# Performance work log

Measured on AMD Instinct MI355X. Metric: run time of the kernel, lower is better.

## Reference

```python
import jax, jax.numpy as jnp
import numpy as np
import math

# Dims chosen per input_specs
B, Q, S, T = 8, 64, 64, 64          # batch, queries, stat (segment) count, tokens per segment
H, DH = 8, 64                        # heads, head dim
NH = H * DH                          # num_hiddens = 512
STAT_K, TOKEN_K = 8, 16
NEG = -1e6


def setup_inputs() -> dict:
    key = jax.random.key(0)
    ks = jax.random.split(key, 11)
    f = lambda k, sh: jax.random.normal(k, sh, dtype=jnp.float32)
    w = lambda k: f(k, (NH, NH)) * 0.05  # Linear weights stored as [in, out]
    return {
        "queries": f(ks[0], (B, Q, NH)),
        "stat_keys": f(ks[1], (B, S, NH)),
        "token_keys": f(ks[2], (B * S, T, NH)),
        "values": f(ks[3], (B * S, T, NH)),
        "stat_valid_lens": jax.random.randint(ks[4], (B,), 1, S + 1, dtype=jnp.int32),
        "Wq_stat": w(ks[5]),
        "Wq_token": w(ks[6]),
        "Wk_stat": w(ks[7]),
        "Wk_token": w(ks[8]),
        "Wv": w(ks[9]),
        "Wo": w(ks[10]),
    }


def reference(queries, stat_keys, token_keys, values, stat_valid_lens,
              Wq_stat, Wq_token, Wk_stat, Wk_token, Wv, Wo):
    scale = 1.0 / math.sqrt(DH)

    def split_heads(x):  # [b, L, H*DH] -> [b, H, L, DH]
        b, L, _ = x.shape
        return x.reshape(b, L, H, DH).transpose(0, 2, 1, 3)

    q_stat = split_heads(queries @ Wq_stat)        # [B,H,Q,DH]
    q_tok = split_heads(queries @ Wq_token)        # [B,H,Q,DH]
    k_stat = split_heads(stat_keys @ Wk_stat)      # [B,H,S,DH]
    # token_keys/values come in as [B*S, T, size]; per-head layout [B,H,S,T,DH]
    k_tok = (token_keys @ Wk_token).reshape(B, S, T, H, DH).transpose(0, 3, 1, 2, 4)
    v = (values @ Wv).reshape(B, S, T, H, DH).transpose(0, 3, 1, 2, 4)

    # --- stat-level scores, valid-length mask, top-k sparsification, softmax ---
    stat_scores = jnp.einsum('bhqd,bhsd->bhqs', q_stat, k_stat) * scale  # [B,H,Q,S]
    valid = jnp.arange(S)[None, None, None, :] < stat_valid_lens[:, None, None, None]
    stat_scores = jnp.where(valid, stat_scores, NEG)
    k1 = min(S - 1, STAT_K)
    _, top_idx = jax.lax.top_k(stat_scores, k1)                           # [B,H,Q,k1]
    keep = jax.nn.one_hot(top_idx, S, dtype=stat_scores.dtype).sum(-2) > 0  # [B,H,Q,S]
    stat_w = jax.nn.softmax(jnp.where(keep, stat_scores, NEG), axis=-1)   # [B,H,Q,S]

    # --- token-level scores. NOTE: the original code computes torch.topk but then
    # overwrites with the LAST k2 positions (token_weights[:, :, -k2:] = ...), so the
    # token top-k result is dead code; we faithfully reproduce the last-k2 masking. ---
    tok_scores = jnp.einsum('bhqd,bhstd->bhsqt', q_tok, k_tok) * scale    # [B,H,S,Q,T]
    k2 = min(T - 1, TOKEN_K)
    last_mask = jnp.arange(T) >= (T - k2)
    tok_w = jax.nn.softmax(jnp.where(last_mask, tok_scores, NEG), axis=-1)
    tok_w = tok_w.transpose(0, 1, 3, 2, 4)                                # [B,H,Q,S,T]

    # --- combine hierarchy and attend over values ---
    comb = stat_w[..., None] * tok_w                                      # [B,H,Q,S,T]
    out = jnp.einsum('bhqst,bhstd->bhqd', comb, v)                        # [B,H,Q,DH]
    out = out.transpose(0, 2, 1, 3).reshape(B, Q, NH)
    return out @ Wo
```

## Files before the change

### kernel.cpp

```cpp
#include <hip/hip_runtime.h>
#include <hip/hip_bf16.h>

#define BB 8
#define QQ 64
#define SS 64
#define TT 64
#define HH 8
#define DH 64
#define NHID 512
#define STAT_K 8
#define TOKEN_K 16

typedef short bf16x8 __attribute__((ext_vector_type(8)));
typedef float f32x4 __attribute__((ext_vector_type(4)));

__device__ inline ushort f2bf_rne(float x) {
    union { float f; unsigned u; } v; v.f = x;
    unsigned r = v.u + 0x7fff + ((v.u >> 16) & 1);
    return (ushort)(r >> 16);
}
__device__ inline float bf2f(ushort h) {
    union { unsigned u; float f; } v; v.u = ((unsigned)h) << 16;
    return v.f;
}

__global__ __launch_bounds__(256) void conv_wT(
    const float* w0, const float* w1, const float* w2,
    const float* w3, const float* w4, const float* w5, ushort* dst)
{
    const float* srcs[6] = {w0, w1, w2, w3, w4, w5};
    const float* src = srcs[blockIdx.z];
    ushort* hi = dst + (size_t)blockIdx.z * 524288;
    ushort* lo = hi + 262144;
    __shared__ float t[32][33];
    const int c0 = blockIdx.x * 32, r0 = blockIdx.y * 32;
    const int tx = threadIdx.x & 31, ty = threadIdx.x >> 5;
    #pragma unroll
    for (int i = 0; i < 4; ++i)
        t[ty + 8 * i][tx] = src[(r0 + ty + 8 * i) * 512 + c0 + tx];
    __syncthreads();
    #pragma unroll
    for (int i = 0; i < 4; ++i) {
        float x = t[tx][ty + 8 * i];
        ushort h = f2bf_rne(x);
        int o = (c0 + ty + 8 * i) * 512 + r0 + tx;
        hi[o] = h;
        lo[o] = f2bf_rne(x - bf2f(h));
    }
}

__global__ void conv_split(const float* __restrict__ src,
                           ushort* __restrict__ hi, ushort* __restrict__ lo, int n)
{
    int i = blockIdx.x * blockDim.x + threadIdx.x;
    if (i < n) {
        float x = src[i];
        ushort h = f2bf_rne(x);
        hi[i] = h;
        lo[i] = f2bf_rne(x - bf2f(h));
    }
}

__global__ void conv_tok(const float* __restrict__ src, ushort* __restrict__ dst)
{
    int v = blockIdx.x * blockDim.x + threadIdx.x;
    int r = v >> 7, c = v & 127;
    int seg = r >> 4, tt = r & 15;
    const float4 x = *(const float4*)(src + (size_t)(seg * 64 + 48 + tt) * 512 + c * 4);
    ushort4 o;
    o.x = f2bf_rne(x.x); o.y = f2bf_rne(x.y);
    o.z = f2bf_rne(x.z); o.w = f2bf_rne(x.w);
    *(ushort4*)(dst + (size_t)v * 4) = o;
}

template <bool SPLIT, bool OUT_BF16>
__global__ __launch_bounds__(256) void gemm_mfma(
    const ushort* __restrict__ Ah, const ushort* __restrict__ Al,
    const ushort* __restrict__ Bh, const ushort* __restrict__ Bl,
    void* __restrict__ C, int M, int N, int K)
{
    __shared__ ushort As[SPLIT ? 2 : 1][64][40];
    __shared__ ushort Bs[SPLIT ? 2 : 1][64][40];
    const int tid = threadIdx.x;
    const int row0 = blockIdx.y * 64, col0 = blockIdx.x * 64;
    const int wave = tid >> 6, lane = tid & 63;
    const int wm = wave & 1, wn = wave >> 1;
    const int m16 = lane & 15, quad = lane >> 4;
    const int srow = tid >> 2, schunk = tid & 3;

    f32x4 acc[2][2];
    #pragma unroll
    for (int i = 0; i < 2; ++i)
        #pragma unroll
        for (int j = 0; j < 2; ++j)
            #pragma unroll
            for (int r = 0; r < 4; ++r) acc[i][j][r] = 0.f;

    for (int k0 = 0; k0 < K; k0 += 32) {
        const size_t aoff = (size_t)(row0 + srow) * K + k0 + schunk * 8;
        const size_t boff = (size_t)(col0 + srow) * K + k0 + schunk * 8;
        uint4 a_h = *(const uint4*)(Ah + aoff);
        uint4 b_h = *(const uint4*)(Bh + boff);
        *(uint4*)&As[0][srow][schunk * 8] = a_h;
        *(uint4*)&Bs[0][srow][schunk * 8] = b_h;
        if constexpr (SPLIT) {
            uint4 a_l = *(const uint4*)(Al + aoff);
            uint4 b_l = *(const uint4*)(Bl + boff);
            *(uint4*)&As[1][srow][schunk * 8] = a_l;
            *(uint4*)&Bs[1][srow][schunk * 8] = b_l;
        }
        __syncthreads();

        bf16x8 af[2], bf[2], afl[2], bfl[2];
        #pragma unroll
        for (int i = 0; i < 2; ++i) {
            af[i] = *(const bf16x8*)&As[0][wm * 32 + i * 16 + m16][quad * 8];
            bf[i] = *(const bf16x8*)&Bs[0][wn * 32 + i * 16 + m16][quad * 8];
            if constexpr (SPLIT) {
                afl[i] = *(const bf16x8*)&As[1][wm * 32 + i * 16 + m16][quad * 8];
                bfl[i] = *(const bf16x8*)&Bs[1][wn * 32 + i * 16 + m16][quad * 8];
            }
        }
        #pragma unroll
        for (int i = 0; i < 2; ++i)
            #pragma unroll
            for (int j = 0; j < 2; ++j) {
                acc[i][j] = __builtin_amdgcn_mfma_f32_16x16x32_bf16(af[i], bf[j], acc[i][j], 0, 0, 0);
                if constexpr (SPLIT) {
                    acc[i][j] = __builtin_amdgcn_mfma_f32_16x16x32_bf16(af[i], bfl[j], acc[i][j], 0, 0, 0);
                    acc[i][j] = __builtin_amdgcn_mfma_f32_16x16x32_bf16(afl[i], bf[j], acc[i][j], 0, 0, 0);
                }
            }
        __syncthreads();
    }

    #pragma unroll
    for (int i = 0; i < 2; ++i)
        #pragma unroll
        for (int j = 0; j < 2; ++j) {
            int r0 = row0 + wm * 32 + i * 16 + quad * 4;
            int c = col0 + wn * 32 + j * 16 + m16;
            #pragma unroll
            for (int reg = 0; reg < 4; ++reg) {
                float v = acc[i][j][reg];
                if constexpr (OUT_BF16)
                    ((ushort*)C)[(size_t)(r0 + reg) * N + c] = f2bf_rne(v);
                else
                    ((float*)C)[(size_t)(r0 + reg) * N + c] = v;
            }
        }
}

__global__ __launch_bounds__(64) void stat_topk(
    const float* __restrict__ q_stat, const float* __restrict__ k_stat,
    const int* __restrict__ valid_lens,
    int* __restrict__ sel_idx, float* __restrict__ sel_w)
{
    const int bid = blockIdx.x;
    const int b = bid >> 9;
    const int hq = bid & 511;
    const int h = hq >> 6;
    const int q = hq & 63;
    const int lane = threadIdx.x;

    __shared__ float sq[64];
    sq[lane] = q_stat[(b * QQ + q) * NHID + h * DH + lane];
    __syncthreads();

    const float4* kr = (const float4*)(k_stat + (b * SS + lane) * NHID + h * DH);
    const float4* sq4 = (const float4*)sq;
    float sc = 0.f;
    #pragma unroll
    for (int i = 0; i < 16; ++i) {
        float4 a = sq4[i], kk = kr[i];
        sc += a.x * kk.x + a.y * kk.y + a.z * kk.z + a.w * kk.w;
    }
    sc *= 0.125f;
    if (lane >= valid_lens[b]) sc = -1e6f;

    float my = sc;
    float mv[STAT_K];
    int   mi[STAT_K];
    #pragma unroll
    for (int j = 0; j < STAT_K; ++j) {
        float v = my;
        int idx = lane;
        #pragma unroll
        for (int off = 32; off > 0; off >>= 1) {
            float ov = __shfl_down(v, off);
            int   oi = __shfl_down(idx, off);
            if (ov > v || (ov == v && oi < idx)) { v = ov; idx = oi; }
        }
        v = __shfl(v, 0);
        idx = __shfl(idx, 0);
        mv[j] = v; mi[j] = idx;
        if (lane == idx) my = -3e38f;
    }
    float m0 = mv[0];
    float den = 0.f;
    float w[STAT_K];
    #pragma unroll
    for (int j = 0; j < STAT_K; ++j) { w[j] = __expf(mv[j] - m0); den += w[j]; }
    float inv = 1.f / den;
    if (lane < STAT_K) {
        sel_idx[bid * STAT_K + lane] = mi[lane];
        sel_w[bid * STAT_K + lane]   = w[lane] * inv;
    }
}

__global__ __launch_bounds__(64) void token_attend2(
    const float* __restrict__ q_tok, const ushort* __restrict__ k_tok,
    const ushort* __restrict__ v_proj, const int* __restrict__ sel_idx,
    const float* __restrict__ sel_w, float* __restrict__ ctx)
{
    const int bid = blockIdx.x;
    const int b = bid >> 9, h = (bid >> 6) & 7, q = bid & 63;
    const int lane = threadIdx.x;

    __shared__ float sq[64];
    __shared__ float ssc[16];
    __shared__ int   ssel[STAT_K];
    __shared__ float ssw[STAT_K];

    sq[lane] = q_tok[(size_t)(b * QQ + q) * NHID + h * DH + lane];
    if (lane < STAT_K) {
        ssel[lane] = sel_idx[bid * STAT_K + lane];
        ssw[lane]  = sel_w[bid * STAT_K + lane];
    }
    __syncthreads();

    const int t = lane >> 2, part = lane & 3;
    float acc = 0.f;

    for (int j = 0; j < STAT_K; ++j) {
        const int s = ssel[j];
        const float wseg = ssw[j];
        const size_t rowbase = (size_t)((b * SS + s) * TOKEN_K);

        const uint4* k4 = (const uint4*)(k_tok + (rowbase + t) * NHID + h * DH + part * 16);
        uint4 ka = k4[0], kb = k4[1];
        const float* qb = &sq[part * 16];
        float p = 0.f;
        p += qb[0]  * bf2f((ushort)(ka.x & 0xffff)) + qb[1]  * bf2f((ushort)(ka.x >> 16));
        p += qb[2]  * bf2f((ushort)(ka.y & 0xffff)) + qb[3]  * bf2f((ushort)(ka.y >> 16));
        p += qb[4]  * bf2f((ushort)(ka.z & 0xffff)) + qb[5]  * bf2f((ushort)(ka.z >> 16));
        p += qb[6]  * bf2f((ushort)(ka.w & 0xffff)) + qb[7]  * bf2f((ushort)(ka.w >> 16));
        p += qb[8]  * bf2f((ushort)(kb.x & 0xffff)) + qb[9]  * bf2f((ushort)(kb.x >> 16));
        p += qb[10] * bf2f((ushort)(kb.y & 0xffff)) + qb[11] * bf2f((ushort)(kb.y >> 16));
        p += qb[12] * bf2f((ushort)(kb.z & 0xffff)) + qb[13] * bf2f((ushort)(kb.z >> 16));
        p += qb[14] * bf2f((ushort)(kb.w & 0xffff)) + qb[15] * bf2f((ushort)(kb.w >> 16));
        p += __shfl_xor(p, 1);
        p += __shfl_xor(p, 2);
        if (part == 0) ssc[t] = p * 0.125f;
        __syncthreads();

        float m = ssc[0];
        #pragma unroll
        for (int tt = 1; tt < TOKEN_K; ++tt) m = fmaxf(m, ssc[tt]);
        float den = 0.f, wv[TOKEN_K];
        #pragma unroll
        for (int tt = 0; tt < TOKEN_K; ++tt) { wv[tt] = __expf(ssc[tt] - m); den += wv[tt]; }

        const ushort* vrow = v_proj + rowbase * NHID + h * DH + lane;
        float loc = 0.f;
        #pragma unroll
        for (int tt = 0; tt < TOKEN_K; ++tt) loc += wv[tt] * bf2f(vrow[tt * NHID]);
        acc += (wseg / den) * loc;
        __syncthreads();
    }

    ctx[(size_t)(b * QQ + q) * NHID + h * DH + lane] = acc;
}

extern "C" void kernel_launch(void* const* d_in, const int* in_sizes, int n_in,
                              void* d_out, int out_size, void* d_ws, size_t ws_size,
                              hipStream_t stream) {
    const float* queries    = (const float*)d_in[0];
    const float* stat_keys  = (const float*)d_in[1];
    const float* token_keys = (const float*)d_in[2];
    const float* values     = (const float*)d_in[3];
    const int*   valid_lens = (const int*)d_in[4];
    const float* Wq_stat    = (const float*)d_in[5];
    const float* Wq_token   = (const float*)d_in[6];
    const float* Wk_stat    = (const float*)d_in[7];
    const float* Wk_token   = (const float*)d_in[8];
    const float* Wv         = (const float*)d_in[9];
    const float* Wo         = (const float*)d_in[10];

    char* w = (char*)d_ws;
    ushort* wT      = (ushort*)(w + 0);
    ushort* q_hi    = (ushort*)(w + 6291456);
    ushort* q_lo    = q_hi + 262144;
    ushort* sk_hi   = (ushort*)(w + 7340032);
    ushort* sk_lo   = sk_hi + 262144;
    float*  q_stat  = (float*)(w + 8388608);
    float*  k_stat  = (float*)(w + 9437184);
    float*  q_tokf  = (float*)(w + 10485760);
    ushort* tok_hi  = (ushort*)(w + 11534336);
    ushort* k_tok   = (ushort*)(w + 19922944);
    ushort* v_projp = (ushort*)(w + 28311552);
    float*  ctx     = (float*)(w + 36700160);
    ushort* ctx_hi  = (ushort*)(w + 37748736);
    ushort* ctx_lo  = ctx_hi + 262144;
    float*  sel_w   = (float*)(w + 38797312);
    int*    sel_idx = (int*)(w + 38928384);

    ushort* wqs_h = wT + 0 * 524288, *wqs_l = wqs_h + 262144;
    ushort* wks_h = wT + 1 * 524288, *wks_l = wks_h + 262144;
    ushort* wqt_h = wT + 2 * 524288, *wqt_l = wqt_h + 262144;
    ushort* wkt_h = wT + 3 * 524288;
    ushort* wv_h  = wT + 4 * 524288;
    ushort* wo_h  = wT + 5 * 524288, *wo_l = wo_h + 262144;

    conv_wT<<<dim3(16, 16, 6), 256, 0, stream>>>(
        Wq_stat, Wk_stat, Wq_token, Wk_token, Wv, Wo, wT);
    conv_split<<<1024, 256, 0, stream>>>(queries, q_hi, q_lo, 262144);
    conv_split<<<1024, 256, 0, stream>>>(stat_keys, sk_hi, sk_lo, 262144);

    gemm_mfma<true, false><<<dim3(8, 8), 256, 0, stream>>>(
        q_hi, q_lo, wqs_h, wqs_l, q_stat, 512, 512, 512);
    gemm_mfma<true, false><<<dim3(8, 8), 256, 0, stream>>>(
        sk_hi, sk_lo, wks_h, wks_l, k_stat, 512, 512, 512);
    gemm_mfma<true, false><<<dim3(8, 8), 256, 0, stream>>>(
        q_hi, q_lo, wqt_h, wqt_l, q_tokf, 512, 512, 512);
    stat_topk<<<4096, 64, 0, stream>>>(q_stat, k_stat, valid_lens, sel_idx, sel_w);

    conv_tok<<<4096, 256, 0, stream>>>(token_keys, tok_hi);
    gemm_mfma<false, true><<<dim3(8, 128), 256, 0, stream>>>(
        tok_hi, nullptr, wkt_h, nullptr, k_tok, 8192, 512, 512);
    conv_tok<<<4096, 256, 0, stream>>>(values, tok_hi);
    gemm_mfma<false, true><<<dim3(8, 128), 256, 0, stream>>>(
        tok_hi, nullptr, wv_h, nullptr, v_projp, 8192, 512, 512);

    token_attend2<<<4096, 64, 0, stream>>>(q_tokf, k_tok, v_projp,
                                           sel_idx, sel_w, ctx);

    conv_split<<<1024, 256, 0, stream>>>(ctx, ctx_hi, ctx_lo, 262144);
    gemm_mfma<true, false><<<dim3(8, 8), 256, 0, stream>>>(
        ctx_hi, ctx_lo, wo_h, wo_l, (float*)d_out, 512, 512, 512);
}
```

Before: 270.0 us.

## Fuse conversion kernels into GEMMs and batch projection launches

Merges the weight transpose and the query/stat-key hi/lo splits into one launch, and batches the three split-precision projection GEMMs into a single grid using the z dimension. The token key/value conversion moves inside a combined GEMM that reads fp32 rows directly and converts them to bf16 while staging into shared memory. The ctx hi/lo split is folded into the attention epilogue. Together these cut the launch count from 14 to 6 and drop the intermediate bf16 token buffers and the fp32 ctx round trip. The cost is extra conversion work inside the GEMM inner loop and fp32 loads that read twice as many bytes.

```diff
diff --git a/kernel.cpp b/kernel.cpp
--- a/kernel.cpp
+++ b/kernel.cpp
@@ -24,63 +24,66 @@
     return v.f;
 }
 
-__global__ __launch_bounds__(256) void conv_wT(
+__global__ __launch_bounds__(256) void conv_all(
     const float* w0, const float* w1, const float* w2,
-    const float* w3, const float* w4, const float* w5, ushort* dst)
-{
-    const float* srcs[6] = {w0, w1, w2, w3, w4, w5};
-    const float* src = srcs[blockIdx.z];
-    ushort* hi = dst + (size_t)blockIdx.z * 524288;
-    ushort* lo = hi + 262144;
-    __shared__ float t[32][33];
-    const int c0 = blockIdx.x * 32, r0 = blockIdx.y * 32;
-    const int tx = threadIdx.x & 31, ty = threadIdx.x >> 5;
-    #pragma unroll
-    for (int i = 0; i < 4; ++i)
-        t[ty + 8 * i][tx] = src[(r0 + ty + 8 * i) * 512 + c0 + tx];
-    __syncthreads();
-    #pragma unroll
-    for (int i = 0; i < 4; ++i) {
-        float x = t[tx][ty + 8 * i];
-        ushort h = f2bf_rne(x);
-        int o = (c0 + ty + 8 * i) * 512 + r0 + tx;
-        hi[o] = h;
-        lo[o] = f2bf_rne(x - bf2f(h));
-    }
-}
-
-__global__ void conv_split(const float* __restrict__ src,
-                           ushort* __restrict__ hi, ushort* __restrict__ lo, int n)
-{
-    int i = blockIdx.x * blockDim.x + threadIdx.x;
-    if (i < n) {
-        float x = src[i];
-        ushort h = f2bf_rne(x);
-        hi[i] = h;
-        lo[i] = f2bf_rne(x - bf2f(h));
-    }
-}
-
-__global__ void conv_tok(const float* __restrict__ src, ushort* __restrict__ dst)
-{
-    int v = blockIdx.x * blockDim.x + threadIdx.x;
-    int r = v >> 7, c = v & 127;
-    int seg = r >> 4, tt = r & 15;
-    const float4 x = *(const float4*)(src + (size_t)(seg * 64 + 48 + tt) * 512 + c * 4);
-    ushort4 o;
-    o.x = f2bf_rne(x.x); o.y = f2bf_rne(x.y);
-    o.z = f2bf_rne(x.z); o.w = f2bf_rne(x.w);
-    *(ushort4*)(dst + (size_t)v * 4) = o;
-}
-
-template <bool SPLIT, bool OUT_BF16>
-__global__ __launch_bounds__(256) void gemm_mfma(
-    const ushort* __restrict__ Ah, const ushort* __restrict__ Al,
-    const ushort* __restrict__ Bh, const ushort* __restrict__ Bl,
-    void* __restrict__ C, int M, int N, int K)
-{
-    __shared__ ushort As[SPLIT ? 2 : 1][64][40];
-    __shared__ ushort Bs[SPLIT ? 2 : 1][64][40];
+    const float* w3, const float* w4, const float* w5,
+    const float* queries, const float* stat_keys,
+    ushort* wT, ushort* q_hi, ushort* q_lo, ushort* sk_hi, ushort* sk_lo)
+{
+    const int z = blockIdx.z;
+    if (z < 6) {
+        const float* srcs[6] = {w0, w1, w2, w3, w4, w5};
+        const float* src = srcs[z];
+        ushort* hi = wT + (size_t)z * 524288;
+        ushort* lo = hi + 262144;
+        __shared__ float t[32][33];
+        const int c0 = blockIdx.x * 32, r0 = blockIdx.y * 32;
+        const int tx = threadIdx.x & 31, ty = threadIdx.x >> 5;
+        #pragma unroll
+        for (int i = 0; i < 4; ++i)
+            t[ty + 8 * i][tx] = src[(r0 + ty + 8 * i) * 512 + c0 + tx];
+        __syncthreads();
+        #pragma unroll
+        for (int i = 0; i < 4; ++i) {
+            float x = t[tx][ty + 8 * i];
+            ushort h = f2bf_rne(x);
+            int o = (c0 + ty + 8 * i) * 512 + r0 + tx;
+            hi[o] = h;
+            lo[o] = f2bf_rne(x - bf2f(h));
+        }
+    } else {
+        const float* src = (z == 6) ? queries : stat_keys;
+        ushort* hi = (z == 6) ? q_hi : sk_hi;
+        ushort* lo = (z == 6) ? q_lo : sk_lo;
+        int base = (blockIdx.y * 16 + blockIdx.x) * 1024 + threadIdx.x * 4;
+        float4 x = *(const float4*)(src + base);
+        ushort4 h, l;
+        h.x = f2bf_rne(x.x); l.x = f2bf_rne(x.x - bf2f(h.x));
+        h.y = f2bf_rne(x.y); l.y = f2bf_rne(x.y - bf2f(h.y));
+        h.z = f2bf_rne(x.z); l.z = f2bf_rne(x.z - bf2f(h.z));
+        h.w = f2bf_rne(x.w); l.w = f2bf_rne(x.w - bf2f(h.w));
+        *(ushort4*)(hi + base) = h;
+        *(ushort4*)(lo + base) = l;
+    }
+}
+
+__global__ __launch_bounds__(256) void gemm_split3(
+    const ushort* __restrict__ q_hi, const ushort* __restrict__ q_lo,
+    const ushort* __restrict__ sk_hi, const ushort* __restrict__ sk_lo,
+    const ushort* __restrict__ wT,
+    float* __restrict__ q_stat, float* __restrict__ k_stat,
+    float* __restrict__ q_tokf)
+{
+    const int z = blockIdx.z;
+    const ushort* Ah = (z == 1) ? sk_hi : q_hi;
+    const ushort* Al = (z == 1) ? sk_lo : q_lo;
+    const ushort* Bh = wT + (size_t)z * 524288;
+    const ushort* Bl = Bh + 262144;
+    float* C = (z == 0) ? q_stat : (z == 1) ? k_stat : q_tokf;
+    const int K = 512, N = 512;
+
+    __shared__ ushort As[2][64][40];
+    __shared__ ushort Bs[2][64][40];
     const int tid = threadIdx.x;
     const int row0 = blockIdx.y * 64, col0 = blockIdx.x * 64;
     const int wave = tid >> 6, lane = tid & 63;
@@ -99,37 +102,27 @@
     for (int k0 = 0; k0 < K; k0 += 32) {
         const size_t aoff = (size_t)(row0 + srow) * K + k0 + schunk * 8;
         const size_t boff = (size_t)(col0 + srow) * K + k0 + schunk * 8;
-        uint4 a_h = *(const uint4*)(Ah + aoff);
-        uint4 b_h = *(const uint4*)(Bh + boff);
-        *(uint4*)&As[0][srow][schunk * 8] = a_h;
-        *(uint4*)&Bs[0][srow][schunk * 8] = b_h;
-        if constexpr (SPLIT) {
-            uint4 a_l = *(const uint4*)(Al + aoff);
-            uint4 b_l = *(const uint4*)(Bl + boff);
-            *(uint4*)&As[1][srow][schunk * 8] = a_l;
-            *(uint4*)&Bs[1][srow][schunk * 8] = b_l;
-        }
+        *(uint4*)&As[0][srow][schunk * 8] = *(const uint4*)(Ah + aoff);
+        *(uint4*)&Bs[0][srow][schunk * 8] = *(const uint4*)(Bh + boff);
+        *(uint4*)&As[1][srow][schunk * 8] = *(const uint4*)(Al + aoff);
+        *(uint4*)&Bs[1][srow][schunk * 8] = *(const uint4*)(Bl + boff);
         __syncthreads();
 
         bf16x8 af[2], bf[2], afl[2], bfl[2];
         #pragma unroll
         for (int i = 0; i < 2; ++i) {
-            af[i] = *(const bf16x8*)&As[0][wm * 32 + i * 16 + m16][quad * 8];
-            bf[i] = *(const bf16x8*)&Bs[0][wn * 32 + i * 16 + m16][quad * 8];
-            if constexpr (SPLIT) {
-                afl[i] = *(const bf16x8*)&As[1][wm * 32 + i * 16 + m16][quad * 8];
-                bfl[i] = *(const bf16x8*)&Bs[1][wn * 32 + i * 16 + m16][quad * 8];
-            }
+            af[i]  = *(const bf16x8*)&As[0][wm * 32 + i * 16 + m16][quad * 8];
+            bf[i]  = *(const bf16x8*)&Bs[0][wn * 32 + i * 16 + m16][quad * 8];
+            afl[i] = *(const bf16x8*)&As[1][wm * 32 + i * 16 + m16][quad * 8];
+            bfl[i] = *(const bf16x8*)&Bs[1][wn * 32 + i * 16 + m16][quad * 8];
         }
         #pragma unroll
         for (int i = 0; i < 2; ++i)
             #pragma unroll
             for (int j = 0; j < 2; ++j) {
                 acc[i][j] = __builtin_amdgcn_mfma_f32_16x16x32_bf16(af[i], bf[j], acc[i][j], 0, 0, 0);
-                if constexpr (SPLIT) {
-                    acc[i][j] = __builtin_amdgcn_mfma_f32_16x16x32_bf16(af[i], bfl[j], acc[i][j], 0, 0, 0);
-                    acc[i][j] = __builtin_amdgcn_mfma_f32_16x16x32_bf16(afl[i], bf[j], acc[i][j], 0, 0, 0);
-                }
+                acc[i][j] = __builtin_amdgcn_mfma_f32_16x16x32_bf16(af[i], bfl[j], acc[i][j], 0, 0, 0);
+                acc[i][j] = __builtin_amdgcn_mfma_f32_16x16x32_bf16(afl[i], bf[j], acc[i][j], 0, 0, 0);
             }
         __syncthreads();
     }
@@ -141,13 +134,143 @@
             int r0 = row0 + wm * 32 + i * 16 + quad * 4;
             int c = col0 + wn * 32 + j * 16 + m16;
             #pragma unroll
-            for (int reg = 0; reg < 4; ++reg) {
-                float v = acc[i][j][reg];
-                if constexpr (OUT_BF16)
-                    ((ushort*)C)[(size_t)(r0 + reg) * N + c] = f2bf_rne(v);
-                else
-                    ((float*)C)[(size_t)(r0 + reg) * N + c] = v;
+            for (int reg = 0; reg < 4; ++reg)
+                C[(size_t)(r0 + reg) * N + c] = acc[i][j][reg];
+        }
+}
+
+__global__ __launch_bounds__(256) void gemm_out(
+    const ushort* __restrict__ Ah, const ushort* __restrict__ Al,
+    const ushort* __restrict__ Bh, const ushort* __restrict__ Bl,
+    float* __restrict__ C)
+{
+    const int K = 512, N = 512;
+    __shared__ ushort As[2][64][40];
+    __shared__ ushort Bs[2][64][40];
+    const int tid = threadIdx.x;
+    const int row0 = blockIdx.y * 64, col0 = blockIdx.x * 64;
+    const int wave = tid >> 6, lane = tid & 63;
+    const int wm = wave & 1, wn = wave >> 1;
+    const int m16 = lane & 15, quad = lane >> 4;
+    const int srow = tid >> 2, schunk = tid & 3;
+
+    f32x4 acc[2][2];
+    #pragma unroll
+    for (int i = 0; i < 2; ++i)
+        #pragma unroll
+        for (int j = 0; j < 2; ++j)
+            #pragma unroll
+            for (int r = 0; r < 4; ++r) acc[i][j][r] = 0.f;
+
+    for (int k0 = 0; k0 < K; k0 += 32) {
+        const size_t aoff = (size_t)(row0 + srow) * K + k0 + schunk * 8;
+        const size_t boff = (size_t)(col0 + srow) * K + k0 + schunk * 8;
+        *(uint4*)&As[0][srow][schunk * 8] = *(const uint4*)(Ah + aoff);
+        *(uint4*)&Bs[0][srow][schunk * 8] = *(const uint4*)(Bh + boff);
+        *(uint4*)&As[1][srow][schunk * 8] = *(const uint4*)(Al + aoff);
+        *(uint4*)&Bs[1][srow][schunk * 8] = *(const uint4*)(Bl + boff);
+        __syncthreads();
+
+        bf16x8 af[2], bf[2], afl[2], bfl[2];
+        #pragma unroll
+        for (int i = 0; i < 2; ++i) {
+            af[i]  = *(const bf16x8*)&As[0][wm * 32 + i * 16 + m16][quad * 8];
+            bf[i]  = *(const bf16x8*)&Bs[0][wn * 32 + i * 16 + m16][quad * 8];
+            afl[i] = *(const bf16x8*)&As[1][wm * 32 + i * 16 + m16][quad * 8];
+            bfl[i] = *(const bf16x8*)&Bs[1][wn * 32 + i * 16 + m16][quad * 8];
+        }
+        #pragma unroll
+        for (int i = 0; i < 2; ++i)
+            #pragma unroll
+            for (int j = 0; j < 2; ++j) {
+                acc[i][j] = __builtin_amdgcn_mfma_f32_16x16x32_bf16(af[i], bf[j], acc[i][j], 0, 0, 0);
+                acc[i][j] = __builtin_amdgcn_mfma_f32_16x16x32_bf16(af[i], bfl[j], acc[i][j], 0, 0, 0);
+                acc[i][j] = __builtin_amdgcn_mfma_f32_16x16x32_bf16(afl[i], bf[j], acc[i][j], 0, 0, 0);
             }
+        __syncthreads();
+    }
+
+    #pragma unroll
+    for (int i = 0; i < 2; ++i)
+        #pragma unroll
+        for (int j = 0; j < 2; ++j) {
+            int r0 = row0 + wm * 32 + i * 16 + quad * 4;
+            int c = col0 + wn * 32 + j * 16 + m16;
+            #pragma unroll
+            for (int reg = 0; reg < 4; ++reg)
+                C[(size_t)(r0 + reg) * N + c] = acc[i][j][reg];
+        }
+}
+
+__global__ __launch_bounds__(256) void gemm_tok(
+    const float* __restrict__ token_keys, const float* __restrict__ values,
+    const ushort* __restrict__ wkt_h, const ushort* __restrict__ wv_h,
+    ushort* __restrict__ k_tok, ushort* __restrict__ v_proj)
+{
+    const int z = blockIdx.z;
+    const float* A = z ? values : token_keys;
+    const ushort* Bh = z ? wv_h : wkt_h;
+    ushort* C = z ? v_proj : k_tok;
+    const int K = 512, N = 512;
+
+    __shared__ ushort As[64][40];
+    __shared__ ushort Bs[64][40];
+    const int tid = threadIdx.x;
+    const int row0 = blockIdx.y * 64, col0 = blockIdx.x * 64;
+    const int wave = tid >> 6, lane = tid & 63;
+    const int wm = wave & 1, wn = wave >> 1;
+    const int m16 = lane & 15, quad = lane >> 4;
+    const int srow = tid >> 2, schunk = tid & 3;
+
+    const int r = row0 + srow;
+    const size_t arow = (size_t)((r >> 4) * 64 + 48 + (r & 15)) * K;
+
+    f32x4 acc[2][2];
+    #pragma unroll
+    for (int i = 0; i < 2; ++i)
+        #pragma unroll
+        for (int j = 0; j < 2; ++j)
+            #pragma unroll
+            for (int rr = 0; rr < 4; ++rr) acc[i][j][rr] = 0.f;
+
+    for (int k0 = 0; k0 < K; k0 += 32) {
+        const float* ap = A + arow + k0 + schunk * 8;
+        float4 x0 = ((const float4*)ap)[0];
+        float4 x1 = ((const float4*)ap)[1];
+        ushort4 h0, h1;
+        h0.x = f2bf_rne(x0.x); h0.y = f2bf_rne(x0.y);
+        h0.z = f2bf_rne(x0.z); h0.w = f2bf_rne(x0.w);
+        h1.x = f2bf_rne(x1.x); h1.y = f2bf_rne(x1.y);
+        h1.z = f2bf_rne(x1.z); h1.w = f2bf_rne(x1.w);
+        *(ushort4*)&As[srow][schunk * 8] = h0;
+        *(ushort4*)&As[srow][schunk * 8 + 4] = h1;
+        *(uint4*)&Bs[srow][schunk * 8] =
+            *(const uint4*)(Bh + (size_t)(col0 + srow) * K + k0 + schunk * 8);
+        __syncthreads();
+
+        bf16x8 af[2], bf[2];
+        #pragma unroll
+        for (int i = 0; i < 2; ++i) {
+            af[i] = *(const bf16x8*)&As[wm * 32 + i * 16 + m16][quad * 8];
+            bf[i] = *(const bf16x8*)&Bs[wn * 32 + i * 16 + m16][quad * 8];
+        }
+        #pragma unroll
+        for (int i = 0; i < 2; ++i)
+            #pragma unroll
+            for (int j = 0; j < 2; ++j)
+                acc[i][j] = __builtin_amdgcn_mfma_f32_16x16x32_bf16(af[i], bf[j], acc[i][j], 0, 0, 0);
+        __syncthreads();
+    }
+
+    #pragma unroll
+    for (int i = 0; i < 2; ++i)
+        #pragma unroll
+        for (int j = 0; j < 2; ++j) {
+            int r0 = row0 + wm * 32 + i * 16 + quad * 4;
+            int c = col0 + wn * 32 + j * 16 + m16;
+            #pragma unroll
+            for (int reg = 0; reg < 4; ++reg)
+                C[(size_t)(r0 + reg) * N + c] = f2bf_rne(acc[i][j][reg]);
         }
 }
 
@@ -211,7 +334,8 @@
 __global__ __launch_bounds__(64) void token_attend2(
     const float* __restrict__ q_tok, const ushort* __restrict__ k_tok,
     const ushort* __restrict__ v_proj, const int* __restrict__ sel_idx,
-    const float* __restrict__ sel_w, float* __restrict__ ctx)
+    const float* __restrict__ sel_w,
+    ushort* __restrict__ ctx_hi, ushort* __restrict__ ctx_lo)
 {
     const int bid = blockIdx.x;
     const int b = bid >> 9, h = (bid >> 6) & 7, q = bid & 63;
@@ -269,7 +393,10 @@
         __syncthreads();
     }
 
-    ctx[(size_t)(b * QQ + q) * NHID + h * DH + lane] = acc;
+    const size_t o = (size_t)(b * QQ + q) * NHID + h * DH + lane;
+    ushort hh = f2bf_rne(acc);
+    ctx_hi[o] = hh;
+    ctx_lo[o] = f2bf_rne(acc - bf2f(hh));
 }
 
 extern "C" void kernel_launch(void* const* d_in, const int* in_sizes, int n_in,
@@ -296,46 +423,32 @@
     float*  q_stat  = (float*)(w + 8388608);
     float*  k_stat  = (float*)(w + 9437184);
     float*  q_tokf  = (float*)(w + 10485760);
-    ushort* tok_hi  = (ushort*)(w + 11534336);
-    ushort* k_tok   = (ushort*)(w + 19922944);
-    ushort* v_projp = (ushort*)(w + 28311552);
-    float*  ctx     = (float*)(w + 36700160);
-    ushort* ctx_hi  = (ushort*)(w + 37748736);
+    ushort* k_tok   = (ushort*)(w + 11534336);
+    ushort* v_projp = (ushort*)(w + 19922944);
+    ushort* ctx_hi  = (ushort*)(w + 28311552);
     ushort* ctx_lo  = ctx_hi + 262144;
-    float*  sel_w   = (float*)(w + 38797312);
-    int*    sel_idx = (int*)(w + 38928384);
-
-    ushort* wqs_h = wT + 0 * 524288, *wqs_l = wqs_h + 262144;
-    ushort* wks_h = wT + 1 * 524288, *wks_l = wks_h + 262144;
-    ushort* wqt_h = wT + 2 * 524288, *wqt_l = wqt_h + 262144;
+    float*  sel_w   = (float*)(w + 29360128);
+    int*    sel_idx = (int*)(w + 29491200);
+
     ushort* wkt_h = wT + 3 * 524288;
     ushort* wv_h  = wT + 4 * 524288;
     ushort* wo_h  = wT + 5 * 524288, *wo_l = wo_h + 262144;
 
-    conv_wT<<<dim3(16, 16, 6), 256, 0, stream>>>(
-        Wq_stat, Wk_stat, Wq_token, Wk_token, Wv, Wo, wT);
-    conv_split<<<1024, 256, 0, stream>>>(queries, q_hi, q_lo, 262144);
-    conv_split<<<1024, 256, 0, stream>>>(stat_keys, sk_hi, sk_lo, 262144);
-
-    gemm_mfma<true, false><<<dim3(8, 8), 256, 0, stream>>>(
-        q_hi, q_lo, wqs_h, wqs_l, q_stat, 512, 512, 512);
-    gemm_mfma<true, false><<<dim3(8, 8), 256, 0, stream>>>(
-        sk_hi, sk_lo, wks_h, wks_l, k_stat, 512, 512, 512);
-    gemm_mfma<true, false><<<dim3(8, 8), 256, 0, stream>>>(
-        q_hi, q_lo, wqt_h, wqt_l, q_tokf, 512, 512, 512);
+    conv_all<<<dim3(16, 16, 8), 256, 0, stream>>>(
+        Wq_stat, Wk_stat, Wq_token, Wk_token, Wv, Wo,
+        queries, stat_keys, wT, q_hi, q_lo, sk_hi, sk_lo);
+
+    gemm_split3<<<dim3(8, 8, 3), 256, 0, stream>>>(
+        q_hi, q_lo, sk_hi, sk_lo, wT, q_stat, k_stat, q_tokf);
+
     stat_topk<<<4096, 64, 0, stream>>>(q_stat, k_stat, valid_lens, sel_idx, sel_w);
 
-    conv_tok<<<4096, 256, 0, stream>>>(token_keys, tok_hi);
-    gemm_mfma<false, true><<<dim3(8, 128), 256, 0, stream>>>(
-        tok_hi, nullptr, wkt_h, nullptr, k_tok, 8192, 512, 512);
-    conv_tok<<<4096, 256, 0, stream>>>(values, tok_hi);
-    gemm_mfma<false, true><<<dim3(8, 128), 256, 0, stream>>>(
-        tok_hi, nullptr, wv_h, nullptr, v_projp, 8192, 512, 512);
+    gemm_tok<<<dim3(8, 128, 2), 256, 0, stream>>>(
+        token_keys, values, wkt_h, wv_h, k_tok, v_projp);
 
     token_attend2<<<4096, 64, 0, stream>>>(q_tokf, k_tok, v_projp,
-                                           sel_idx, sel_w, ctx);
-
-    conv_split<<<1024, 256, 0, stream>>>(ctx, ctx_hi, ctx_lo, 262144);
-    gemm_mfma<true, false><<<dim3(8, 8), 256, 0, stream>>>(
-        ctx_hi, ctx_lo, wo_h, wo_l, (float*)d_out, 512, 512, 512);
-}
+                                           sel_idx, sel_w, ctx_hi, ctx_lo);
+
+    gemm_out<<<dim3(8, 8), 256, 0, stream>>>(
+        ctx_hi, ctx_lo, wo_h, wo_l, (float*)d_out);
+}
```

After: 239.9 us. 11.1% less time.
